# Kernel tuning notes

Measured on AMD Instinct MI355X. Metric: run time of the kernel, lower is better.

## Reference

```python
import jax, jax.numpy as jnp
import numpy as np

EPS = 1e-6

def setup_inputs() -> dict:
    key = jax.random.key(0)
    ks = jax.random.split(key, 8)
    D = 64
    x = jax.random.normal(ks[0], (32, 56, 56, 4 * D), jnp.float32)
    beta = jnp.zeros((1, 1, 1, 4 * D), jnp.float32)
    diag = lambda k: 0.5 + 0.1 * jax.random.uniform(k, (D,), jnp.float32)
    off = lambda k: 0.05 * jax.random.normal(k, (D,), jnp.float32)
    k2 = jax.random.split(ks[1], 10)
    return dict(
        x=x, beta=beta,
        gam_rr=diag(k2[0]), gam_ri=off(k2[1]), gam_rj=off(k2[2]), gam_rk=off(k2[3]),
        gam_ii=diag(k2[4]), gam_ij=off(k2[5]), gam_ik=off(k2[6]),
        gam_jj=diag(k2[7]), gam_jk=off(k2[8]), gam_kk=diag(k2[9]),
    )

def _hbn(x, beta, gam_rr, gam_ri, gam_rj, gam_rk, gam_ii, gam_ij, gam_ik, gam_jj, gam_jk, gam_kk):
    # Training-mode quaternion/tessarine whitening BN (activation_position='after').
    N, H, W, C = x.shape
    d = C // 4
    mean = jnp.mean(x, axis=(0, 1, 2))           # [C]
    c = x - mean
    r, i, j, k = jnp.split(c, 4, axis=-1)        # each [N,H,W,d]
    m = lambda a, b: jnp.mean(a * b, axis=(0, 1, 2))  # [d]
    Vrr = m(r, r) + EPS; Vri = m(r, i); Vrj = m(r, j); Vrk = m(r, k)
    Vii = m(i, i) + EPS; Vij = m(i, j); Vik = m(i, k)
    Vjj = m(j, j) + EPS; Vjk = m(j, k); Vkk = m(k, k) + EPS
    # Symmetric 4x4 covariance per channel -> [d,4,4]
    V = jnp.stack([
        jnp.stack([Vrr, Vri, Vrj, Vrk], -1),
        jnp.stack([Vri, Vii, Vij, Vik], -1),
        jnp.stack([Vrj, Vij, Vjj, Vjk], -1),
        jnp.stack([Vrk, Vik, Vjk, Vkk], -1)], -2)
    # Whitening matrix W = V^{-1/2} (ZCA) via symmetric eigendecomposition
    w, U = jnp.linalg.eigh(V)
    Wm = jnp.einsum('dab,db,dcb->dac', U, 1.0 / jnp.sqrt(w), U)  # [d,4,4]
    v = jnp.stack([r, i, j, k], axis=-1)         # [N,H,W,d,4]
    xh = jnp.einsum('dec,nhwdc->nhwde', Wm, v)   # whitened components
    # 10-parameter symmetric affine recombination
    G = jnp.stack([
        jnp.stack([gam_rr, gam_ri, gam_rj, gam_rk], -1),
        jnp.stack([gam_ri, gam_ii, gam_ij, gam_ik], -1),
        jnp.stack([gam_rj, gam_ij, gam_jj, gam_jk], -1),
        jnp.stack([gam_rk, gam_ik, gam_jk, gam_kk], -1)], -2)  # [d,4,4]
    y = jnp.einsum('dec,nhwdc->nhwde', G, xh)
    y = jnp.concatenate([y[..., 0], y[..., 1], y[..., 2], y[..., 3]], axis=-1) + beta
    return jax.nn.elu(y)

def reference(x, beta, gam_rr, gam_ri, gam_rj, gam_rk, gam_ii, gam_ij, gam_ik, gam_jj, gam_jk, gam_kk):
    return _hbn(x, beta, gam_rr, gam_ri, gam_rj, gam_rk, gam_ii, gam_ij, gam_ik, gam_jj, gam_jk, gam_kk)
```

## Files before the change

kernel.cpp:

```cpp
#include <hip/hip_runtime.h>
#include <math.h>

static constexpr int NPOS = 32 * 56 * 56;
static constexpr int CCH  = 256;
static constexpr int NB   = 256;
static constexpr double EPSV = 1e-6;


__global__ __launch_bounds__(1024) void hbn_reduce(const float* __restrict__ x,
                                                   float* __restrict__ partial) {
  const int tid  = threadIdx.x;
  const int lane = tid & 63;
  const int gw   = blockIdx.x * (1024 >> 6) + (tid >> 6);
  const int nw   = NB * (1024 >> 6);

  float s0=0.f, s1=0.f, s2=0.f, s3=0.f;
  float q0=0.f,q1=0.f,q2=0.f,q3=0.f,q4=0.f,q5=0.f,q6=0.f,q7=0.f,q8=0.f,q9=0.f;

  for (int p = gw * 2; p < NPOS; p += nw * 2) {
    const float* b = x + (size_t)p * CCH + lane;
    float r0 = b[0],   i0 = b[64],  j0 = b[128], k0 = b[192];
    float r1 = b[256], i1 = b[320], j1 = b[384], k1 = b[448];
    s0 += r0 + r1; s1 += i0 + i1; s2 += j0 + j1; s3 += k0 + k1;
    q0 = fmaf(r0,r0, fmaf(r1,r1, q0));
    q1 = fmaf(r0,i0, fmaf(r1,i1, q1));
    q2 = fmaf(r0,j0, fmaf(r1,j1, q2));
    q3 = fmaf(r0,k0, fmaf(r1,k1, q3));
    q4 = fmaf(i0,i0, fmaf(i1,i1, q4));
    q5 = fmaf(i0,j0, fmaf(i1,j1, q5));
    q6 = fmaf(i0,k0, fmaf(i1,k1, q6));
    q7 = fmaf(j0,j0, fmaf(j1,j1, q7));
    q8 = fmaf(j0,k0, fmaf(j1,k1, q8));
    q9 = fmaf(k0,k0, fmaf(k1,k1, q9));
  }

  __shared__ float red[14][1024];
  red[0][tid]=s0;  red[1][tid]=s1;  red[2][tid]=s2;  red[3][tid]=s3;
  red[4][tid]=q0;  red[5][tid]=q1;  red[6][tid]=q2;  red[7][tid]=q3;
  red[8][tid]=q4;  red[9][tid]=q5;  red[10][tid]=q6; red[11][tid]=q7;
  red[12][tid]=q8; red[13][tid]=q9;
  __syncthreads();
  if (tid < 64) {
    float* dst = partial + (size_t)blockIdx.x * 896;
#pragma unroll
    for (int q = 0; q < 14; ++q) {
      float v = 0.f;
#pragma unroll
      for (int w = 0; w < 16; ++w) v += red[q][tid + 64*w];
      dst[q*64 + tid] = v;
    }
  }
}

__global__ __launch_bounds__(256) void hbn_sum(const float* __restrict__ partial,
                                               double* __restrict__ S) {
  const int t = blockIdx.x * 256 + threadIdx.x;
  if (t >= 896) return;
  double acc = 0.0;
#pragma unroll 8
  for (int b = 0; b < NB; ++b) acc += (double)partial[(size_t)b * 896 + t];
  S[t] = acc;
}

__global__ void hbn_solve(const double* __restrict__ S,
                          const float* __restrict__ beta,
                          const float* __restrict__ grr, const float* __restrict__ gri,
                          const float* __restrict__ grj, const float* __restrict__ grk,
                          const float* __restrict__ gii, const float* __restrict__ gij,
                          const float* __restrict__ gik, const float* __restrict__ gjj,
                          const float* __restrict__ gjk, const float* __restrict__ gkk,
                          float* __restrict__ Mmat, float* __restrict__ offv) {
  const int d = threadIdx.x;
  const double invM = 1.0 / (double)NPOS;

  double mu[4];
  mu[0] = S[0*64+d]*invM; mu[1] = S[1*64+d]*invM;
  mu[2] = S[2*64+d]*invM; mu[3] = S[3*64+d]*invM;

  float A[4][4];
  A[0][0] = (float)(S[4*64+d]*invM  - mu[0]*mu[0] + EPSV);
  A[0][1] = A[1][0] = (float)(S[5*64+d]*invM  - mu[0]*mu[1]);
  A[0][2] = A[2][0] = (float)(S[6*64+d]*invM  - mu[0]*mu[2]);
  A[0][3] = A[3][0] = (float)(S[7*64+d]*invM  - mu[0]*mu[3]);
  A[1][1] = (float)(S[8*64+d]*invM  - mu[1]*mu[1] + EPSV);
  A[1][2] = A[2][1] = (float)(S[9*64+d]*invM  - mu[1]*mu[2]);
  A[1][3] = A[3][1] = (float)(S[10*64+d]*invM - mu[1]*mu[3]);
  A[2][2] = (float)(S[11*64+d]*invM - mu[2]*mu[2] + EPSV);
  A[2][3] = A[3][2] = (float)(S[12*64+d]*invM - mu[2]*mu[3]);
  A[3][3] = (float)(S[13*64+d]*invM - mu[3]*mu[3] + EPSV);

  float U[4][4] = {{1,0,0,0},{0,1,0,0},{0,0,1,0},{0,0,0,1}};

#pragma unroll 1
  for (int sweep = 0; sweep < 6; ++sweep) {
#pragma unroll
    for (int p = 0; p < 3; ++p) {
#pragma unroll
      for (int q = p + 1; q < 4; ++q) {
        float apq = A[p][q];
        if (fabsf(apq) > 1e-30f) {
          float theta = (A[q][q] - A[p][p]) / (2.0f * apq);
          float t = 1.0f / (fabsf(theta) + sqrtf(fmaf(theta, theta, 1.0f)));
          if (theta < 0.0f) t = -t;
          float c = rsqrtf(fmaf(t, t, 1.0f));
          float s = t * c;
#pragma unroll
          for (int r = 0; r < 4; ++r) {
            float arp = A[r][p], arq = A[r][q];
            A[r][p] = c*arp - s*arq;  A[r][q] = s*arp + c*arq;
          }
#pragma unroll
          for (int r = 0; r < 4; ++r) {
            float apr = A[p][r], aqr = A[q][r];
            A[p][r] = c*apr - s*aqr;  A[q][r] = s*apr + c*aqr;
          }
#pragma unroll
          for (int r = 0; r < 4; ++r) {
            float urp = U[r][p], urq = U[r][q];
            U[r][p] = c*urp - s*urq;  U[r][q] = s*urp + c*urq;
          }
        }
      }
    }
  }

  float wis[4];
#pragma unroll
  for (int b = 0; b < 4; ++b) {
    float w = A[b][b];
    if (w < 1e-12f) w = 1e-12f;
    wis[b] = rsqrtf(w);
  }

  float Wm[4][4];
#pragma unroll
  for (int a = 0; a < 4; ++a)
#pragma unroll
    for (int cc = 0; cc < 4; ++cc) {
      float acc = 0.0f;
#pragma unroll
      for (int b = 0; b < 4; ++b) acc += U[a][b] * wis[b] * U[cc][b];
      Wm[a][cc] = acc;
    }

  float G[4][4];
  G[0][0] = grr[d]; G[0][1] = G[1][0] = gri[d];
  G[0][2] = G[2][0] = grj[d]; G[0][3] = G[3][0] = grk[d];
  G[1][1] = gii[d]; G[1][2] = G[2][1] = gij[d];
  G[1][3] = G[3][1] = gik[d];
  G[2][2] = gjj[d]; G[2][3] = G[3][2] = gjk[d];
  G[3][3] = gkk[d];

  float M[4][4];
#pragma unroll
  for (int e = 0; e < 4; ++e)
#pragma unroll
    for (int cc = 0; cc < 4; ++cc) {
      float acc = 0.0f;
#pragma unroll
      for (int b = 0; b < 4; ++b) acc += G[e][b] * Wm[b][cc];
      M[e][cc] = acc;
      Mmat[d*16 + e*4 + cc] = acc;
    }

#pragma unroll
  for (int e = 0; e < 4; ++e) {
    float acc = beta[e*64 + d];
#pragma unroll
    for (int cc = 0; cc < 4; ++cc) acc -= M[e][cc] * (float)mu[cc];
    offv[e*64 + d] = acc;
  }
}

__global__ __launch_bounds__(256) void hbn_apply(const float* __restrict__ x,
                                                 const float* __restrict__ Mmat,
                                                 const float* __restrict__ offv,
                                                 float* __restrict__ out) {
  const int tid  = threadIdx.x;
  const int lane = tid & 63;
  const int gw   = blockIdx.x * (blockDim.x >> 6) + (tid >> 6);
  const int nw   = gridDim.x * (blockDim.x >> 6);

  const float m0  = Mmat[lane*16+0],  m1  = Mmat[lane*16+1],  m2  = Mmat[lane*16+2],  m3  = Mmat[lane*16+3];
  const float m4  = Mmat[lane*16+4],  m5  = Mmat[lane*16+5],  m6  = Mmat[lane*16+6],  m7  = Mmat[lane*16+7];
  const float m8  = Mmat[lane*16+8],  m9  = Mmat[lane*16+9],  m10 = Mmat[lane*16+10], m11 = Mmat[lane*16+11];
  const float m12 = Mmat[lane*16+12], m13 = Mmat[lane*16+13], m14 = Mmat[lane*16+14], m15 = Mmat[lane*16+15];
  const float o0 = offv[lane], o1 = offv[64+lane], o2 = offv[128+lane], o3 = offv[192+lane];

  for (int p = gw * 2; p < NPOS; p += nw * 2) {
    const float* b = x + (size_t)p * CCH + lane;
    float r0 = b[0],   i0 = b[64],  j0 = b[128], k0 = b[192];
    float r1 = b[256], i1 = b[320], j1 = b[384], k1 = b[448];

    float ya0 = fmaf(m0, r0, fmaf(m1, i0, fmaf(m2, j0, fmaf(m3, k0, o0))));
    float ya1 = fmaf(m4, r0, fmaf(m5, i0, fmaf(m6, j0, fmaf(m7, k0, o1))));
    float ya2 = fmaf(m8, r0, fmaf(m9, i0, fmaf(m10,j0, fmaf(m11,k0, o2))));
    float ya3 = fmaf(m12,r0, fmaf(m13,i0, fmaf(m14,j0, fmaf(m15,k0, o3))));
    float yb0 = fmaf(m0, r1, fmaf(m1, i1, fmaf(m2, j1, fmaf(m3, k1, o0))));
    float yb1 = fmaf(m4, r1, fmaf(m5, i1, fmaf(m6, j1, fmaf(m7, k1, o1))));
    float yb2 = fmaf(m8, r1, fmaf(m9, i1, fmaf(m10,j1, fmaf(m11,k1, o2))));
    float yb3 = fmaf(m12,r1, fmaf(m13,i1, fmaf(m14,j1, fmaf(m15,k1, o3))));

    ya0 = ya0 > 0.f ? ya0 : (__expf(ya0) - 1.f);
    ya1 = ya1 > 0.f ? ya1 : (__expf(ya1) - 1.f);
    ya2 = ya2 > 0.f ? ya2 : (__expf(ya2) - 1.f);
    ya3 = ya3 > 0.f ? ya3 : (__expf(ya3) - 1.f);
    yb0 = yb0 > 0.f ? yb0 : (__expf(yb0) - 1.f);
    yb1 = yb1 > 0.f ? yb1 : (__expf(yb1) - 1.f);
    yb2 = yb2 > 0.f ? yb2 : (__expf(yb2) - 1.f);
    yb3 = yb3 > 0.f ? yb3 : (__expf(yb3) - 1.f);

    float* ob = out + (size_t)p * CCH + lane;
    __builtin_nontemporal_store(ya0, ob + 0);
    __builtin_nontemporal_store(ya1, ob + 64);
    __builtin_nontemporal_store(ya2, ob + 128);
    __builtin_nontemporal_store(ya3, ob + 192);
    __builtin_nontemporal_store(yb0, ob + 256);
    __builtin_nontemporal_store(yb1, ob + 320);
    __builtin_nontemporal_store(yb2, ob + 384);
    __builtin_nontemporal_store(yb3, ob + 448);
  }
}

extern "C" void kernel_launch(void* const* d_in, const int* in_sizes, int n_in,
                              void* d_out, int out_size, void* d_ws, size_t ws_size,
                              hipStream_t stream) {
  (void)in_sizes; (void)n_in; (void)out_size; (void)ws_size;
  const float* x    = (const float*)d_in[0];
  const float* beta = (const float*)d_in[1];
  const float* grr  = (const float*)d_in[2];
  const float* gri  = (const float*)d_in[3];
  const float* grj  = (const float*)d_in[4];
  const float* grk  = (const float*)d_in[5];
  const float* gii  = (const float*)d_in[6];
  const float* gij  = (const float*)d_in[7];
  const float* gik  = (const float*)d_in[8];
  const float* gjj  = (const float*)d_in[9];
  const float* gjk  = (const float*)d_in[10];
  const float* gkk  = (const float*)d_in[11];
  float* out = (float*)d_out;

  double* S      = (double*)d_ws;
  float*  Mmat   = (float*)((char*)d_ws + 7168);
  float*  offv   = (float*)((char*)d_ws + 11264);
  float*  partial= (float*)((char*)d_ws + 12288);

  hbn_reduce<<<NB, 1024, 0, stream>>>(x, partial);
  hbn_sum<<<4, 256, 0, stream>>>(partial, S);
  hbn_solve<<<1, 64, 0, stream>>>(S, beta, grr, gri, grj, grk,
                                  gii, gij, gik, gjj, gjk, gkk, Mmat, offv);
  hbn_apply<<<2048, 256, 0, stream>>>(x, Mmat, offv, out);
}
```

Baseline: 76.93 us.

## Fuse reduce, solve and apply into one cooperative kernel with grid syncs

Replaces the four-kernel pipeline with a single cooperative kernel of 1024 blocks. It accumulates statistics, grid-syncs, sums the partials in double with wave shuffles, grid-syncs again, and then has every block redundantly solve the 64 per-channel 4x4 whitening matrices into shared memory before the apply pass. The aim is to remove launch gaps and the single-block solve stall between passes. The costs are two grid-wide barriers, redundant per-block solve work, and a dependence on co-residency of 1024 blocks; a fallback multi-kernel path with the reduce grid halved is kept for when the workspace is too small or the cooperative launch fails.

```diff
diff --git a/kernel.cpp b/kernel.cpp
--- a/kernel.cpp
+++ b/kernel.cpp
@@ -1,22 +1,253 @@
 #include <hip/hip_runtime.h>
+#include <hip/hip_cooperative_groups.h>
 #include <math.h>
 
-static constexpr int NPOS = 32 * 56 * 56;
-static constexpr int CCH  = 256;
-static constexpr int NB   = 256;
+namespace cg = cooperative_groups;
+
+static constexpr int NPOS  = 32 * 56 * 56;
+static constexpr int CCH   = 256;
+static constexpr int FGRID = 1024;
 static constexpr double EPSV = 1e-6;
 
 
-__global__ __launch_bounds__(1024) void hbn_reduce(const float* __restrict__ x,
-                                                   float* __restrict__ partial) {
+__device__ __forceinline__ void solve_one(const double* __restrict__ S,
+                                          const float* __restrict__ beta,
+                                          const float* __restrict__ grr, const float* __restrict__ gri,
+                                          const float* __restrict__ grj, const float* __restrict__ grk,
+                                          const float* __restrict__ gii, const float* __restrict__ gij,
+                                          const float* __restrict__ gik, const float* __restrict__ gjj,
+                                          const float* __restrict__ gjk, const float* __restrict__ gkk,
+                                          int d, float* Mout , float* offout ) {
+  const double invM = 1.0 / (double)NPOS;
+  double mu[4];
+  mu[0] = S[0*64+d]*invM; mu[1] = S[1*64+d]*invM;
+  mu[2] = S[2*64+d]*invM; mu[3] = S[3*64+d]*invM;
+
+  float A[4][4];
+  A[0][0] = (float)(S[4*64+d]*invM  - mu[0]*mu[0] + EPSV);
+  A[0][1] = A[1][0] = (float)(S[5*64+d]*invM  - mu[0]*mu[1]);
+  A[0][2] = A[2][0] = (float)(S[6*64+d]*invM  - mu[0]*mu[2]);
+  A[0][3] = A[3][0] = (float)(S[7*64+d]*invM  - mu[0]*mu[3]);
+  A[1][1] = (float)(S[8*64+d]*invM  - mu[1]*mu[1] + EPSV);
+  A[1][2] = A[2][1] = (float)(S[9*64+d]*invM  - mu[1]*mu[2]);
+  A[1][3] = A[3][1] = (float)(S[10*64+d]*invM - mu[1]*mu[3]);
+  A[2][2] = (float)(S[11*64+d]*invM - mu[2]*mu[2] + EPSV);
+  A[2][3] = A[3][2] = (float)(S[12*64+d]*invM - mu[2]*mu[3]);
+  A[3][3] = (float)(S[13*64+d]*invM - mu[3]*mu[3] + EPSV);
+
+  float U[4][4] = {{1,0,0,0},{0,1,0,0},{0,0,1,0},{0,0,0,1}};
+
+#pragma unroll 1
+  for (int sweep = 0; sweep < 6; ++sweep) {
+#pragma unroll
+    for (int p = 0; p < 3; ++p) {
+#pragma unroll
+      for (int q = p + 1; q < 4; ++q) {
+        float apq = A[p][q];
+        if (fabsf(apq) > 1e-30f) {
+          float theta = (A[q][q] - A[p][p]) / (2.0f * apq);
+          float t = 1.0f / (fabsf(theta) + sqrtf(fmaf(theta, theta, 1.0f)));
+          if (theta < 0.0f) t = -t;
+          float c = rsqrtf(fmaf(t, t, 1.0f));
+          float s = t * c;
+#pragma unroll
+          for (int r = 0; r < 4; ++r) {
+            float arp = A[r][p], arq = A[r][q];
+            A[r][p] = c*arp - s*arq;  A[r][q] = s*arp + c*arq;
+          }
+#pragma unroll
+          for (int r = 0; r < 4; ++r) {
+            float apr = A[p][r], aqr = A[q][r];
+            A[p][r] = c*apr - s*aqr;  A[q][r] = s*apr + c*aqr;
+          }
+#pragma unroll
+          for (int r = 0; r < 4; ++r) {
+            float urp = U[r][p], urq = U[r][q];
+            U[r][p] = c*urp - s*urq;  U[r][q] = s*urp + c*urq;
+          }
+        }
+      }
+    }
+  }
+
+  float wis[4];
+#pragma unroll
+  for (int b = 0; b < 4; ++b) {
+    float w = A[b][b];
+    if (w < 1e-12f) w = 1e-12f;
+    wis[b] = rsqrtf(w);
+  }
+
+  float Wm[4][4];
+#pragma unroll
+  for (int a = 0; a < 4; ++a)
+#pragma unroll
+    for (int cc = 0; cc < 4; ++cc) {
+      float acc = 0.0f;
+#pragma unroll
+      for (int b = 0; b < 4; ++b) acc += U[a][b] * wis[b] * U[cc][b];
+      Wm[a][cc] = acc;
+    }
+
+  float G[4][4];
+  G[0][0] = grr[d]; G[0][1] = G[1][0] = gri[d];
+  G[0][2] = G[2][0] = grj[d]; G[0][3] = G[3][0] = grk[d];
+  G[1][1] = gii[d]; G[1][2] = G[2][1] = gij[d];
+  G[1][3] = G[3][1] = gik[d];
+  G[2][2] = gjj[d]; G[2][3] = G[3][2] = gjk[d];
+  G[3][3] = gkk[d];
+
+  float M[4][4];
+#pragma unroll
+  for (int e = 0; e < 4; ++e)
+#pragma unroll
+    for (int cc = 0; cc < 4; ++cc) {
+      float acc = 0.0f;
+#pragma unroll
+      for (int b = 0; b < 4; ++b) acc += G[e][b] * Wm[b][cc];
+      M[e][cc] = acc;
+      Mout[e*4 + cc] = acc;
+    }
+
+#pragma unroll
+  for (int e = 0; e < 4; ++e) {
+    float acc = beta[e*64 + d];
+#pragma unroll
+    for (int cc = 0; cc < 4; ++cc) acc -= M[e][cc] * (float)mu[cc];
+    offout[e] = acc;
+  }
+}
+
+__global__ __launch_bounds__(256, 4) void hbn_fused(
+    const float* __restrict__ x, const float* __restrict__ beta,
+    const float* __restrict__ grr, const float* __restrict__ gri,
+    const float* __restrict__ grj, const float* __restrict__ grk,
+    const float* __restrict__ gii, const float* __restrict__ gij,
+    const float* __restrict__ gik, const float* __restrict__ gjj,
+    const float* __restrict__ gjk, const float* __restrict__ gkk,
+    float* __restrict__ partial, double* __restrict__ Sg,
+    float* __restrict__ out) {
+  cg::grid_group grid = cg::this_grid();
   const int tid  = threadIdx.x;
   const int lane = tid & 63;
-  const int gw   = blockIdx.x * (1024 >> 6) + (tid >> 6);
-  const int nw   = NB * (1024 >> 6);
+  const int wib  = tid >> 6;
+  const int gw   = blockIdx.x * 4 + wib;
+  const int nw   = FGRID * 4;
+
+  {
+    float s0=0.f, s1=0.f, s2=0.f, s3=0.f;
+    float q0=0.f,q1=0.f,q2=0.f,q3=0.f,q4=0.f,q5=0.f,q6=0.f,q7=0.f,q8=0.f,q9=0.f;
+
+    for (int p = gw * 2; p < NPOS; p += nw * 2) {
+      const float* b = x + (size_t)p * CCH + lane;
+      float r0 = b[0],   i0 = b[64],  j0 = b[128], k0 = b[192];
+      float r1 = b[256], i1 = b[320], j1 = b[384], k1 = b[448];
+      s0 += r0 + r1; s1 += i0 + i1; s2 += j0 + j1; s3 += k0 + k1;
+      q0 = fmaf(r0,r0, fmaf(r1,r1, q0));
+      q1 = fmaf(r0,i0, fmaf(r1,i1, q1));
+      q2 = fmaf(r0,j0, fmaf(r1,j1, q2));
+      q3 = fmaf(r0,k0, fmaf(r1,k1, q3));
+      q4 = fmaf(i0,i0, fmaf(i1,i1, q4));
+      q5 = fmaf(i0,j0, fmaf(i1,j1, q5));
+      q6 = fmaf(i0,k0, fmaf(i1,k1, q6));
+      q7 = fmaf(j0,j0, fmaf(j1,j1, q7));
+      q8 = fmaf(j0,k0, fmaf(j1,k1, q8));
+      q9 = fmaf(k0,k0, fmaf(k1,k1, q9));
+    }
+
+    __shared__ float red[14][256];
+    red[0][tid]=s0;  red[1][tid]=s1;  red[2][tid]=s2;  red[3][tid]=s3;
+    red[4][tid]=q0;  red[5][tid]=q1;  red[6][tid]=q2;  red[7][tid]=q3;
+    red[8][tid]=q4;  red[9][tid]=q5;  red[10][tid]=q6; red[11][tid]=q7;
+    red[12][tid]=q8; red[13][tid]=q9;
+    __syncthreads();
+    if (tid < 64) {
+      float* dst = partial + (size_t)blockIdx.x * 896;
+#pragma unroll
+      for (int q = 0; q < 14; ++q) {
+        float v = red[q][tid] + red[q][tid+64] + red[q][tid+128] + red[q][tid+192];
+        dst[q*64 + tid] = v;
+      }
+    }
+  }
+  grid.sync();
+
+  if (gw < 896) {
+    double acc = 0.0;
+#pragma unroll
+    for (int m = 0; m < FGRID / 64; ++m)
+      acc += (double)partial[(size_t)(m * 64 + lane) * 896 + gw];
+#pragma unroll
+    for (int off = 32; off > 0; off >>= 1) acc += __shfl_down(acc, off);
+    if (lane == 0) Sg[gw] = acc;
+  }
+  grid.sync();
+
+  __shared__ float Ms[64 * 16];
+  __shared__ float offs[256];
+  if (tid < 64) {
+    float Mo[16], oo[4];
+    solve_one(Sg, beta, grr, gri, grj, grk, gii, gij, gik, gjj, gjk, gkk,
+              tid, Mo, oo);
+#pragma unroll
+    for (int c = 0; c < 16; ++c) Ms[tid*16 + c] = Mo[c];
+#pragma unroll
+    for (int e = 0; e < 4; ++e) offs[e*64 + tid] = oo[e];
+  }
+  __syncthreads();
+
+  const float m0  = Ms[lane*16+0],  m1  = Ms[lane*16+1],  m2  = Ms[lane*16+2],  m3  = Ms[lane*16+3];
+  const float m4  = Ms[lane*16+4],  m5  = Ms[lane*16+5],  m6  = Ms[lane*16+6],  m7  = Ms[lane*16+7];
+  const float m8  = Ms[lane*16+8],  m9  = Ms[lane*16+9],  m10 = Ms[lane*16+10], m11 = Ms[lane*16+11];
+  const float m12 = Ms[lane*16+12], m13 = Ms[lane*16+13], m14 = Ms[lane*16+14], m15 = Ms[lane*16+15];
+  const float o0 = offs[lane], o1 = offs[64+lane], o2 = offs[128+lane], o3 = offs[192+lane];
+
+  for (int p = gw * 2; p < NPOS; p += nw * 2) {
+    const float* b = x + (size_t)p * CCH + lane;
+    float r0 = b[0],   i0 = b[64],  j0 = b[128], k0 = b[192];
+    float r1 = b[256], i1 = b[320], j1 = b[384], k1 = b[448];
+
+    float ya0 = fmaf(m0, r0, fmaf(m1, i0, fmaf(m2, j0, fmaf(m3, k0, o0))));
+    float ya1 = fmaf(m4, r0, fmaf(m5, i0, fmaf(m6, j0, fmaf(m7, k0, o1))));
+    float ya2 = fmaf(m8, r0, fmaf(m9, i0, fmaf(m10,j0, fmaf(m11,k0, o2))));
+    float ya3 = fmaf(m12,r0, fmaf(m13,i0, fmaf(m14,j0, fmaf(m15,k0, o3))));
+    float yb0 = fmaf(m0, r1, fmaf(m1, i1, fmaf(m2, j1, fmaf(m3, k1, o0))));
+    float yb1 = fmaf(m4, r1, fmaf(m5, i1, fmaf(m6, j1, fmaf(m7, k1, o1))));
+    float yb2 = fmaf(m8, r1, fmaf(m9, i1, fmaf(m10,j1, fmaf(m11,k1, o2))));
+    float yb3 = fmaf(m12,r1, fmaf(m13,i1, fmaf(m14,j1, fmaf(m15,k1, o3))));
+
+    ya0 = ya0 > 0.f ? ya0 : (__expf(ya0) - 1.f);
+    ya1 = ya1 > 0.f ? ya1 : (__expf(ya1) - 1.f);
+    ya2 = ya2 > 0.f ? ya2 : (__expf(ya2) - 1.f);
+    ya3 = ya3 > 0.f ? ya3 : (__expf(ya3) - 1.f);
+    yb0 = yb0 > 0.f ? yb0 : (__expf(yb0) - 1.f);
+    yb1 = yb1 > 0.f ? yb1 : (__expf(yb1) - 1.f);
+    yb2 = yb2 > 0.f ? yb2 : (__expf(yb2) - 1.f);
+    yb3 = yb3 > 0.f ? yb3 : (__expf(yb3) - 1.f);
+
+    float* ob = out + (size_t)p * CCH + lane;
+    __builtin_nontemporal_store(ya0, ob + 0);
+    __builtin_nontemporal_store(ya1, ob + 64);
+    __builtin_nontemporal_store(ya2, ob + 128);
+    __builtin_nontemporal_store(ya3, ob + 192);
+    __builtin_nontemporal_store(yb0, ob + 256);
+    __builtin_nontemporal_store(yb1, ob + 320);
+    __builtin_nontemporal_store(yb2, ob + 384);
+    __builtin_nontemporal_store(yb3, ob + 448);
+  }
+}
+
+static constexpr int NBF = 128;
+
+__global__ __launch_bounds__(1024) void fb_reduce(const float* __restrict__ x,
+                                                  float* __restrict__ partial) {
+  const int tid  = threadIdx.x;
+  const int lane = tid & 63;
+  const int gw   = blockIdx.x * 16 + (tid >> 6);
+  const int nw   = NBF * 16;
 
   float s0=0.f, s1=0.f, s2=0.f, s3=0.f;
   float q0=0.f,q1=0.f,q2=0.f,q3=0.f,q4=0.f,q5=0.f,q6=0.f,q7=0.f,q8=0.f,q9=0.f;
-
   for (int p = gw * 2; p < NPOS; p += nw * 2) {
     const float* b = x + (size_t)p * CCH + lane;
     float r0 = b[0],   i0 = b[64],  j0 = b[128], k0 = b[192];
@@ -33,7 +264,6 @@
     q8 = fmaf(j0,k0, fmaf(j1,k1, q8));
     q9 = fmaf(k0,k0, fmaf(k1,k1, q9));
   }
-
   __shared__ float red[14][1024];
   red[0][tid]=s0;  red[1][tid]=s1;  red[2][tid]=s2;  red[3][tid]=s3;
   red[4][tid]=q0;  red[5][tid]=q1;  red[6][tid]=q2;  red[7][tid]=q3;
@@ -52,134 +282,40 @@
   }
 }
 
-__global__ __launch_bounds__(256) void hbn_sum(const float* __restrict__ partial,
-                                               double* __restrict__ S) {
+__global__ __launch_bounds__(256) void fb_sum(const float* __restrict__ partial,
+                                              double* __restrict__ S) {
   const int t = blockIdx.x * 256 + threadIdx.x;
   if (t >= 896) return;
   double acc = 0.0;
 #pragma unroll 8
-  for (int b = 0; b < NB; ++b) acc += (double)partial[(size_t)b * 896 + t];
+  for (int b = 0; b < NBF; ++b) acc += (double)partial[(size_t)b * 896 + t];
   S[t] = acc;
 }
 
-__global__ void hbn_solve(const double* __restrict__ S,
-                          const float* __restrict__ beta,
-                          const float* __restrict__ grr, const float* __restrict__ gri,
-                          const float* __restrict__ grj, const float* __restrict__ grk,
-                          const float* __restrict__ gii, const float* __restrict__ gij,
-                          const float* __restrict__ gik, const float* __restrict__ gjj,
-                          const float* __restrict__ gjk, const float* __restrict__ gkk,
-                          float* __restrict__ Mmat, float* __restrict__ offv) {
+__global__ void fb_solve(const double* __restrict__ S, const float* __restrict__ beta,
+                         const float* __restrict__ grr, const float* __restrict__ gri,
+                         const float* __restrict__ grj, const float* __restrict__ grk,
+                         const float* __restrict__ gii, const float* __restrict__ gij,
+                         const float* __restrict__ gik, const float* __restrict__ gjj,
+                         const float* __restrict__ gjk, const float* __restrict__ gkk,
+                         float* __restrict__ Mmat, float* __restrict__ offv) {
   const int d = threadIdx.x;
-  const double invM = 1.0 / (double)NPOS;
-
-  double mu[4];
-  mu[0] = S[0*64+d]*invM; mu[1] = S[1*64+d]*invM;
-  mu[2] = S[2*64+d]*invM; mu[3] = S[3*64+d]*invM;
-
-  float A[4][4];
-  A[0][0] = (float)(S[4*64+d]*invM  - mu[0]*mu[0] + EPSV);
-  A[0][1] = A[1][0] = (float)(S[5*64+d]*invM  - mu[0]*mu[1]);
-  A[0][2] = A[2][0] = (float)(S[6*64+d]*invM  - mu[0]*mu[2]);
-  A[0][3] = A[3][0] = (float)(S[7*64+d]*invM  - mu[0]*mu[3]);
-  A[1][1] = (float)(S[8*64+d]*invM  - mu[1]*mu[1] + EPSV);
-  A[1][2] = A[2][1] = (float)(S[9*64+d]*invM  - mu[1]*mu[2]);
-  A[1][3] = A[3][1] = (float)(S[10*64+d]*invM - mu[1]*mu[3]);
-  A[2][2] = (float)(S[11*64+d]*invM - mu[2]*mu[2] + EPSV);
-  A[2][3] = A[3][2] = (float)(S[12*64+d]*invM - mu[2]*mu[3]);
-  A[3][3] = (float)(S[13*64+d]*invM - mu[3]*mu[3] + EPSV);
-
-  float U[4][4] = {{1,0,0,0},{0,1,0,0},{0,0,1,0},{0,0,0,1}};
-
-#pragma unroll 1
-  for (int sweep = 0; sweep < 6; ++sweep) {
-#pragma unroll
-    for (int p = 0; p < 3; ++p) {
-#pragma unroll
-      for (int q = p + 1; q < 4; ++q) {
-        float apq = A[p][q];
-        if (fabsf(apq) > 1e-30f) {
-          float theta = (A[q][q] - A[p][p]) / (2.0f * apq);
-          float t = 1.0f / (fabsf(theta) + sqrtf(fmaf(theta, theta, 1.0f)));
-          if (theta < 0.0f) t = -t;
-          float c = rsqrtf(fmaf(t, t, 1.0f));
-          float s = t * c;
-#pragma unroll
-          for (int r = 0; r < 4; ++r) {
-            float arp = A[r][p], arq = A[r][q];
-            A[r][p] = c*arp - s*arq;  A[r][q] = s*arp + c*arq;
-          }
-#pragma unroll
-          for (int r = 0; r < 4; ++r) {
-            float apr = A[p][r], aqr = A[q][r];
-            A[p][r] = c*apr - s*aqr;  A[q][r] = s*apr + c*aqr;
-          }
-#pragma unroll
-          for (int r = 0; r < 4; ++r) {
-            float urp = U[r][p], urq = U[r][q];
-            U[r][p] = c*urp - s*urq;  U[r][q] = s*urp + c*urq;
-          }
-        }
-      }
-    }
-  }
-
-  float wis[4];
-#pragma unroll
-  for (int b = 0; b < 4; ++b) {
-    float w = A[b][b];
-    if (w < 1e-12f) w = 1e-12f;
-    wis[b] = rsqrtf(w);
-  }
-
-  float Wm[4][4];
-#pragma unroll
-  for (int a = 0; a < 4; ++a)
-#pragma unroll
-    for (int cc = 0; cc < 4; ++cc) {
-      float acc = 0.0f;
-#pragma unroll
-      for (int b = 0; b < 4; ++b) acc += U[a][b] * wis[b] * U[cc][b];
-      Wm[a][cc] = acc;
-    }
-
-  float G[4][4];
-  G[0][0] = grr[d]; G[0][1] = G[1][0] = gri[d];
-  G[0][2] = G[2][0] = grj[d]; G[0][3] = G[3][0] = grk[d];
-  G[1][1] = gii[d]; G[1][2] = G[2][1] = gij[d];
-  G[1][3] = G[3][1] = gik[d];
-  G[2][2] = gjj[d]; G[2][3] = G[3][2] = gjk[d];
-  G[3][3] = gkk[d];
-
-  float M[4][4];
-#pragma unroll
-  for (int e = 0; e < 4; ++e)
-#pragma unroll
-    for (int cc = 0; cc < 4; ++cc) {
-      float acc = 0.0f;
-#pragma unroll
-      for (int b = 0; b < 4; ++b) acc += G[e][b] * Wm[b][cc];
-      M[e][cc] = acc;
-      Mmat[d*16 + e*4 + cc] = acc;
-    }
-
-#pragma unroll
-  for (int e = 0; e < 4; ++e) {
-    float acc = beta[e*64 + d];
-#pragma unroll
-    for (int cc = 0; cc < 4; ++cc) acc -= M[e][cc] * (float)mu[cc];
-    offv[e*64 + d] = acc;
-  }
-}
-
-__global__ __launch_bounds__(256) void hbn_apply(const float* __restrict__ x,
-                                                 const float* __restrict__ Mmat,
-                                                 const float* __restrict__ offv,
-                                                 float* __restrict__ out) {
+  float Mo[16], oo[4];
+  solve_one(S, beta, grr, gri, grj, grk, gii, gij, gik, gjj, gjk, gkk, d, Mo, oo);
+#pragma unroll
+  for (int c = 0; c < 16; ++c) Mmat[d*16 + c] = Mo[c];
+#pragma unroll
+  for (int e = 0; e < 4; ++e) offv[e*64 + d] = oo[e];
+}
+
+__global__ __launch_bounds__(256) void fb_apply(const float* __restrict__ x,
+                                                const float* __restrict__ Mmat,
+                                                const float* __restrict__ offv,
+                                                float* __restrict__ out) {
   const int tid  = threadIdx.x;
   const int lane = tid & 63;
-  const int gw   = blockIdx.x * (blockDim.x >> 6) + (tid >> 6);
-  const int nw   = gridDim.x * (blockDim.x >> 6);
+  const int gw   = blockIdx.x * 4 + (tid >> 6);
+  const int nw   = gridDim.x * 4;
 
   const float m0  = Mmat[lane*16+0],  m1  = Mmat[lane*16+1],  m2  = Mmat[lane*16+2],  m3  = Mmat[lane*16+3];
   const float m4  = Mmat[lane*16+4],  m5  = Mmat[lane*16+5],  m6  = Mmat[lane*16+6],  m7  = Mmat[lane*16+7];
@@ -191,7 +327,6 @@
     const float* b = x + (size_t)p * CCH + lane;
     float r0 = b[0],   i0 = b[64],  j0 = b[128], k0 = b[192];
     float r1 = b[256], i1 = b[320], j1 = b[384], k1 = b[448];
-
     float ya0 = fmaf(m0, r0, fmaf(m1, i0, fmaf(m2, j0, fmaf(m3, k0, o0))));
     float ya1 = fmaf(m4, r0, fmaf(m5, i0, fmaf(m6, j0, fmaf(m7, k0, o1))));
     float ya2 = fmaf(m8, r0, fmaf(m9, i0, fmaf(m10,j0, fmaf(m11,k0, o2))));
@@ -200,7 +335,6 @@
     float yb1 = fmaf(m4, r1, fmaf(m5, i1, fmaf(m6, j1, fmaf(m7, k1, o1))));
     float yb2 = fmaf(m8, r1, fmaf(m9, i1, fmaf(m10,j1, fmaf(m11,k1, o2))));
     float yb3 = fmaf(m12,r1, fmaf(m13,i1, fmaf(m14,j1, fmaf(m15,k1, o3))));
-
     ya0 = ya0 > 0.f ? ya0 : (__expf(ya0) - 1.f);
     ya1 = ya1 > 0.f ? ya1 : (__expf(ya1) - 1.f);
     ya2 = ya2 > 0.f ? ya2 : (__expf(ya2) - 1.f);
@@ -209,7 +343,6 @@
     yb1 = yb1 > 0.f ? yb1 : (__expf(yb1) - 1.f);
     yb2 = yb2 > 0.f ? yb2 : (__expf(yb2) - 1.f);
     yb3 = yb3 > 0.f ? yb3 : (__expf(yb3) - 1.f);
-
     float* ob = out + (size_t)p * CCH + lane;
     __builtin_nontemporal_store(ya0, ob + 0);
     __builtin_nontemporal_store(ya1, ob + 64);
@@ -225,7 +358,7 @@
 extern "C" void kernel_launch(void* const* d_in, const int* in_sizes, int n_in,
                               void* d_out, int out_size, void* d_ws, size_t ws_size,
                               hipStream_t stream) {
-  (void)in_sizes; (void)n_in; (void)out_size; (void)ws_size;
+  (void)in_sizes; (void)n_in; (void)out_size;
   const float* x    = (const float*)d_in[0];
   const float* beta = (const float*)d_in[1];
   const float* grr  = (const float*)d_in[2];
@@ -245,9 +378,25 @@
   float*  offv   = (float*)((char*)d_ws + 11264);
   float*  partial= (float*)((char*)d_ws + 12288);
 
-  hbn_reduce<<<NB, 1024, 0, stream>>>(x, partial);
-  hbn_sum<<<4, 256, 0, stream>>>(partial, S);
-  hbn_solve<<<1, 64, 0, stream>>>(S, beta, grr, gri, grj, grk,
-                                  gii, gij, gik, gjj, gjk, gkk, Mmat, offv);
-  hbn_apply<<<2048, 256, 0, stream>>>(x, Mmat, offv, out);
-}
+  const size_t need = 12288 + (size_t)FGRID * 896 * sizeof(float);
+  bool fused_ok = (ws_size >= need);
+
+  if (fused_ok) {
+    void* args[] = { (void*)&x, (void*)&beta,
+                     (void*)&grr, (void*)&gri, (void*)&grj, (void*)&grk,
+                     (void*)&gii, (void*)&gij, (void*)&gik, (void*)&gjj,
+                     (void*)&gjk, (void*)&gkk,
+                     (void*)&partial, (void*)&S, (void*)&out };
+    hipError_t err = hipLaunchCooperativeKernel((const void*)hbn_fused,
+                                                dim3(FGRID), dim3(256),
+                                                args, 0, stream);
+    if (err == hipSuccess) return;
+    (void)hipGetLastError();
+  }
+
+  fb_reduce<<<NBF, 1024, 0, stream>>>(x, partial);
+  fb_sum<<<4, 256, 0, stream>>>(partial, S);
+  fb_solve<<<1, 64, 0, stream>>>(S, beta, grr, gri, grj, grk,
+                                 gii, gij, gik, gjj, gjk, gkk, Mmat, offv);
+  fb_apply<<<2048, 256, 0, stream>>>(x, Mmat, offv, out);
+}
```

New measurement: 287.3 us. 3.74x slower.

## Vectorize reduce and apply with float4 loads and transposed matrix layout

Applied to the files above, without the earlier changes.

Each lane now loads float4 chunks covering 4 channels, and a wavefront covers 4 positions at once, replacing scalar 32-bit loads and stores in both the statistics reduction and the apply pass. The reduction combines results across lanes with shuffles and uses a smaller shared buffer. The whitening matrix is stored transposed so that apply can load its coefficients as vectors. Block counts are also changed. The aim is fewer memory instructions and better bandwidth use. The cost is higher register pressure from 56 accumulators per thread and twice as many partials for hbn_sum to combine.

```diff
diff --git a/kernel.cpp b/kernel.cpp
--- a/kernel.cpp
+++ b/kernel.cpp
@@ -1,55 +1,82 @@
 #include <hip/hip_runtime.h>
 #include <math.h>
 
-static constexpr int NPOS = 32 * 56 * 56;
-static constexpr int CCH  = 256;
-static constexpr int NB   = 256;
+static constexpr int NPOS  = 32 * 56 * 56;
+static constexpr int NQUAD = NPOS / 4;
+static constexpr int CCH   = 256;
+static constexpr int RB    = 512;
+static constexpr int AB    = 1024;
 static constexpr double EPSV = 1e-6;
 
-
-__global__ __launch_bounds__(1024) void hbn_reduce(const float* __restrict__ x,
-                                                   float* __restrict__ partial) {
-  const int tid  = threadIdx.x;
-  const int lane = tid & 63;
-  const int gw   = blockIdx.x * (1024 >> 6) + (tid >> 6);
-  const int nw   = NB * (1024 >> 6);
-
-  float s0=0.f, s1=0.f, s2=0.f, s3=0.f;
-  float q0=0.f,q1=0.f,q2=0.f,q3=0.f,q4=0.f,q5=0.f,q6=0.f,q7=0.f,q8=0.f,q9=0.f;
-
-  for (int p = gw * 2; p < NPOS; p += nw * 2) {
-    const float* b = x + (size_t)p * CCH + lane;
-    float r0 = b[0],   i0 = b[64],  j0 = b[128], k0 = b[192];
-    float r1 = b[256], i1 = b[320], j1 = b[384], k1 = b[448];
-    s0 += r0 + r1; s1 += i0 + i1; s2 += j0 + j1; s3 += k0 + k1;
-    q0 = fmaf(r0,r0, fmaf(r1,r1, q0));
-    q1 = fmaf(r0,i0, fmaf(r1,i1, q1));
-    q2 = fmaf(r0,j0, fmaf(r1,j1, q2));
-    q3 = fmaf(r0,k0, fmaf(r1,k1, q3));
-    q4 = fmaf(i0,i0, fmaf(i1,i1, q4));
-    q5 = fmaf(i0,j0, fmaf(i1,j1, q5));
-    q6 = fmaf(i0,k0, fmaf(i1,k1, q6));
-    q7 = fmaf(j0,j0, fmaf(j1,j1, q7));
-    q8 = fmaf(j0,k0, fmaf(j1,k1, q8));
-    q9 = fmaf(k0,k0, fmaf(k1,k1, q9));
-  }
-
-  __shared__ float red[14][1024];
-  red[0][tid]=s0;  red[1][tid]=s1;  red[2][tid]=s2;  red[3][tid]=s3;
-  red[4][tid]=q0;  red[5][tid]=q1;  red[6][tid]=q2;  red[7][tid]=q3;
-  red[8][tid]=q4;  red[9][tid]=q5;  red[10][tid]=q6; red[11][tid]=q7;
-  red[12][tid]=q8; red[13][tid]=q9;
+typedef float f32x4 __attribute__((ext_vector_type(4)));
+
+
+__device__ __forceinline__ float eluf(float v) {
+  return v > 0.f ? v : (__expf(v) - 1.f);
+}
+
+__global__ __launch_bounds__(256) void hbn_reduce(const float* __restrict__ x,
+                                                  float* __restrict__ partial) {
+  const int tid   = threadIdx.x;
+  const int lane  = tid & 63;
+  const int wib   = tid >> 6;
+  const int psub  = lane >> 4;
+  const int dquad = lane & 15;
+  const int gw    = blockIdx.x * 4 + wib;
+  const int nw    = RB * 4;
+
+  float acc[14][4];
+#pragma unroll
+  for (int s = 0; s < 14; ++s)
+#pragma unroll
+    for (int t = 0; t < 4; ++t) acc[s][t] = 0.f;
+
+  for (int pq = gw; pq < NQUAD; pq += nw) {
+    const float* b = x + (size_t)(pq * 4 + psub) * CCH + dquad * 4;
+    const f32x4 r4 = *reinterpret_cast<const f32x4*>(b);
+    const f32x4 i4 = *reinterpret_cast<const f32x4*>(b + 64);
+    const f32x4 j4 = *reinterpret_cast<const f32x4*>(b + 128);
+    const f32x4 k4 = *reinterpret_cast<const f32x4*>(b + 192);
+#pragma unroll
+    for (int t = 0; t < 4; ++t) {
+      const float r = r4[t], i = i4[t], j = j4[t], k = k4[t];
+      acc[0][t] += r;  acc[1][t] += i;  acc[2][t] += j;  acc[3][t] += k;
+      acc[4][t]  = fmaf(r, r, acc[4][t]);
+      acc[5][t]  = fmaf(r, i, acc[5][t]);
+      acc[6][t]  = fmaf(r, j, acc[6][t]);
+      acc[7][t]  = fmaf(r, k, acc[7][t]);
+      acc[8][t]  = fmaf(i, i, acc[8][t]);
+      acc[9][t]  = fmaf(i, j, acc[9][t]);
+      acc[10][t] = fmaf(i, k, acc[10][t]);
+      acc[11][t] = fmaf(j, j, acc[11][t]);
+      acc[12][t] = fmaf(j, k, acc[12][t]);
+      acc[13][t] = fmaf(k, k, acc[13][t]);
+    }
+  }
+
+#pragma unroll
+  for (int s = 0; s < 14; ++s)
+#pragma unroll
+    for (int t = 0; t < 4; ++t) {
+      float v = acc[s][t];
+      v += __shfl_xor(v, 16);
+      v += __shfl_xor(v, 32);
+      acc[s][t] = v;
+    }
+
+  __shared__ float lds[4][896];
+  if (lane < 16) {
+#pragma unroll
+    for (int s = 0; s < 14; ++s)
+#pragma unroll
+      for (int t = 0; t < 4; ++t)
+        lds[wib][s * 64 + dquad * 4 + t] = acc[s][t];
+  }
   __syncthreads();
-  if (tid < 64) {
-    float* dst = partial + (size_t)blockIdx.x * 896;
-#pragma unroll
-    for (int q = 0; q < 14; ++q) {
-      float v = 0.f;
-#pragma unroll
-      for (int w = 0; w < 16; ++w) v += red[q][tid + 64*w];
-      dst[q*64 + tid] = v;
-    }
-  }
+
+  float* dst = partial + (size_t)blockIdx.x * 896;
+  for (int idx = tid; idx < 896; idx += 256)
+    dst[idx] = lds[0][idx] + lds[1][idx] + lds[2][idx] + lds[3][idx];
 }
 
 __global__ __launch_bounds__(256) void hbn_sum(const float* __restrict__ partial,
@@ -58,7 +85,7 @@
   if (t >= 896) return;
   double acc = 0.0;
 #pragma unroll 8
-  for (int b = 0; b < NB; ++b) acc += (double)partial[(size_t)b * 896 + t];
+  for (int b = 0; b < RB; ++b) acc += (double)partial[(size_t)b * 896 + t];
   S[t] = acc;
 }
 
@@ -69,7 +96,7 @@
                           const float* __restrict__ gii, const float* __restrict__ gij,
                           const float* __restrict__ gik, const float* __restrict__ gjj,
                           const float* __restrict__ gjk, const float* __restrict__ gkk,
-                          float* __restrict__ Mmat, float* __restrict__ offv) {
+                          float* __restrict__ Mt, float* __restrict__ offv) {
   const int d = threadIdx.x;
   const double invM = 1.0 / (double)NPOS;
 
@@ -160,7 +187,7 @@
 #pragma unroll
       for (int b = 0; b < 4; ++b) acc += G[e][b] * Wm[b][cc];
       M[e][cc] = acc;
-      Mmat[d*16 + e*4 + cc] = acc;
+      Mt[(e*4 + cc)*64 + d] = acc;
     }
 
 #pragma unroll
@@ -173,52 +200,47 @@
 }
 
 __global__ __launch_bounds__(256) void hbn_apply(const float* __restrict__ x,
-                                                 const float* __restrict__ Mmat,
+                                                 const float* __restrict__ Mt,
                                                  const float* __restrict__ offv,
                                                  float* __restrict__ out) {
-  const int tid  = threadIdx.x;
-  const int lane = tid & 63;
-  const int gw   = blockIdx.x * (blockDim.x >> 6) + (tid >> 6);
-  const int nw   = gridDim.x * (blockDim.x >> 6);
-
-  const float m0  = Mmat[lane*16+0],  m1  = Mmat[lane*16+1],  m2  = Mmat[lane*16+2],  m3  = Mmat[lane*16+3];
-  const float m4  = Mmat[lane*16+4],  m5  = Mmat[lane*16+5],  m6  = Mmat[lane*16+6],  m7  = Mmat[lane*16+7];
-  const float m8  = Mmat[lane*16+8],  m9  = Mmat[lane*16+9],  m10 = Mmat[lane*16+10], m11 = Mmat[lane*16+11];
-  const float m12 = Mmat[lane*16+12], m13 = Mmat[lane*16+13], m14 = Mmat[lane*16+14], m15 = Mmat[lane*16+15];
-  const float o0 = offv[lane], o1 = offv[64+lane], o2 = offv[128+lane], o3 = offv[192+lane];
-
-  for (int p = gw * 2; p < NPOS; p += nw * 2) {
-    const float* b = x + (size_t)p * CCH + lane;
-    float r0 = b[0],   i0 = b[64],  j0 = b[128], k0 = b[192];
-    float r1 = b[256], i1 = b[320], j1 = b[384], k1 = b[448];
-
-    float ya0 = fmaf(m0, r0, fmaf(m1, i0, fmaf(m2, j0, fmaf(m3, k0, o0))));
-    float ya1 = fmaf(m4, r0, fmaf(m5, i0, fmaf(m6, j0, fmaf(m7, k0, o1))));
-    float ya2 = fmaf(m8, r0, fmaf(m9, i0, fmaf(m10,j0, fmaf(m11,k0, o2))));
-    float ya3 = fmaf(m12,r0, fmaf(m13,i0, fmaf(m14,j0, fmaf(m15,k0, o3))));
-    float yb0 = fmaf(m0, r1, fmaf(m1, i1, fmaf(m2, j1, fmaf(m3, k1, o0))));
-    float yb1 = fmaf(m4, r1, fmaf(m5, i1, fmaf(m6, j1, fmaf(m7, k1, o1))));
-    float yb2 = fmaf(m8, r1, fmaf(m9, i1, fmaf(m10,j1, fmaf(m11,k1, o2))));
-    float yb3 = fmaf(m12,r1, fmaf(m13,i1, fmaf(m14,j1, fmaf(m15,k1, o3))));
-
-    ya0 = ya0 > 0.f ? ya0 : (__expf(ya0) - 1.f);
-    ya1 = ya1 > 0.f ? ya1 : (__expf(ya1) - 1.f);
-    ya2 = ya2 > 0.f ? ya2 : (__expf(ya2) - 1.f);
-    ya3 = ya3 > 0.f ? ya3 : (__expf(ya3) - 1.f);
-    yb0 = yb0 > 0.f ? yb0 : (__expf(yb0) - 1.f);
-    yb1 = yb1 > 0.f ? yb1 : (__expf(yb1) - 1.f);
-    yb2 = yb2 > 0.f ? yb2 : (__expf(yb2) - 1.f);
-    yb3 = yb3 > 0.f ? yb3 : (__expf(yb3) - 1.f);
-
-    float* ob = out + (size_t)p * CCH + lane;
-    __builtin_nontemporal_store(ya0, ob + 0);
-    __builtin_nontemporal_store(ya1, ob + 64);
-    __builtin_nontemporal_store(ya2, ob + 128);
-    __builtin_nontemporal_store(ya3, ob + 192);
-    __builtin_nontemporal_store(yb0, ob + 256);
-    __builtin_nontemporal_store(yb1, ob + 320);
-    __builtin_nontemporal_store(yb2, ob + 384);
-    __builtin_nontemporal_store(yb3, ob + 448);
+  const int tid   = threadIdx.x;
+  const int lane  = tid & 63;
+  const int psub  = lane >> 4;
+  const int dquad = lane & 15;
+  const int gw    = blockIdx.x * 4 + (tid >> 6);
+  const int nw    = AB * 4;
+
+  f32x4 mc[16];
+#pragma unroll
+  for (int c = 0; c < 16; ++c)
+    mc[c] = *reinterpret_cast<const f32x4*>(Mt + c * 64 + dquad * 4);
+  f32x4 ob[4];
+#pragma unroll
+  for (int e = 0; e < 4; ++e)
+    ob[e] = *reinterpret_cast<const f32x4*>(offv + e * 64 + dquad * 4);
+
+  for (int pq = gw; pq < NQUAD; pq += nw) {
+    const size_t pbase = (size_t)(pq * 4 + psub) * CCH + dquad * 4;
+    const float* b = x + pbase;
+    const f32x4 r4 = *reinterpret_cast<const f32x4*>(b);
+    const f32x4 i4 = *reinterpret_cast<const f32x4*>(b + 64);
+    const f32x4 j4 = *reinterpret_cast<const f32x4*>(b + 128);
+    const f32x4 k4 = *reinterpret_cast<const f32x4*>(b + 192);
+
+    float* o = out + pbase;
+#pragma unroll
+    for (int e = 0; e < 4; ++e) {
+      f32x4 y;
+#pragma unroll
+      for (int t = 0; t < 4; ++t)
+        y[t] = fmaf(mc[e*4][t], r4[t],
+               fmaf(mc[e*4+1][t], i4[t],
+               fmaf(mc[e*4+2][t], j4[t],
+               fmaf(mc[e*4+3][t], k4[t], ob[e][t]))));
+#pragma unroll
+      for (int t = 0; t < 4; ++t) y[t] = eluf(y[t]);
+      __builtin_nontemporal_store(y, reinterpret_cast<f32x4*>(o + e * 64));
+    }
   }
 }
 
@@ -241,13 +263,13 @@
   float* out = (float*)d_out;
 
   double* S      = (double*)d_ws;
-  float*  Mmat   = (float*)((char*)d_ws + 7168);
+  float*  Mt     = (float*)((char*)d_ws + 7168);
   float*  offv   = (float*)((char*)d_ws + 11264);
   float*  partial= (float*)((char*)d_ws + 12288);
 
-  hbn_reduce<<<NB, 1024, 0, stream>>>(x, partial);
+  hbn_reduce<<<RB, 256, 0, stream>>>(x, partial);
   hbn_sum<<<4, 256, 0, stream>>>(partial, S);
   hbn_solve<<<1, 64, 0, stream>>>(S, beta, grr, gri, grj, grk,
-                                  gii, gij, gik, gjj, gjk, gkk, Mmat, offv);
-  hbn_apply<<<2048, 256, 0, stream>>>(x, Mmat, offv, out);
-}
+                                  gii, gij, gik, gjj, gjk, gkk, Mt, offv);
+  hbn_apply<<<AB, 256, 0, stream>>>(x, Mt, offv, out);
+}
```

Measured after the change: 91.30 us. +18.7%, slower.
